# Performance work log

Measured on AMD Instinct MI355X. Metric: run time of the kernel, lower is better.

## Reference

```python
import jax, jax.numpy as jnp
import numpy as np

EPS = 1e-6


def _mp_match(reps, att, kernel):
    """BiMPM multi-perspective match.
    reps: (B,L,D); att: (B,L,D) or (B,1,D); kernel: (M,D).
    Returns (B,L,1+M): [tanh(sum(reps*att)), tanh(sum_d reps*kernel_m*att)].
    """
    prod = reps * att                                   # (B,L,D)
    cos = jnp.tanh(jnp.sum(prod, axis=-1, keepdims=True))   # (B,L,1)
    mp = jnp.tanh(jnp.einsum('bld,md->blm', prod, kernel))  # (B,L,M)
    return jnp.concatenate([cos, mp], axis=-1)


def setup_inputs() -> dict:
    key = jax.random.key(0)
    ks = jax.random.split(key, 12)
    B, Llt, Lrt, D, M, A = 32, 128, 128, 512, 64, 128
    H = D // 2
    u = lambda k, shape: jax.random.uniform(k, shape, jnp.float32, -0.05, 0.05)  # keras 'uniform' init
    return {
        'reps_lt': jax.random.normal(ks[0], (B, Llt, D), jnp.float32),
        'h_lt_fw': jax.random.normal(ks[1], (B, H), jnp.float32),
        'h_lt_bw': jax.random.normal(ks[2], (B, H), jnp.float32),
        'reps_rt': jax.random.normal(ks[3], (B, Lrt, D), jnp.float32),
        'h_rt_fw': jax.random.normal(ks[4], (B, H), jnp.float32),
        'h_rt_bw': jax.random.normal(ks[5], (B, H), jnp.float32),
        'kernel_full': u(ks[6], (M, D)),
        'kernel_mpool': u(ks[7], (M, D)),
        'attn_w1': u(ks[8], (D, A)),
        'diag_w': u(ks[9], (A,)),
        'kernel_att': u(ks[10], (M, D)),
        'kernel_maxatt': u(ks[11], (M, D)),
    }


def reference(reps_lt, h_lt_fw, h_lt_bw, reps_rt, h_rt_fw, h_rt_bw,
              kernel_full, kernel_mpool, attn_w1, diag_w,
              kernel_att, kernel_maxatt):
    # ---- full match: each left timestep vs last BiLSTM state of right ----
    h_rt = jnp.concatenate([h_rt_fw, h_rt_bw], axis=-1)[:, None, :]  # (B,1,D)
    full = _mp_match(reps_lt, h_rt, kernel_full)                     # (B,Ll,1+M)

    # ---- max-pooling match ----
    # t[b,r,l,m] = tanh(sum_d R[b,r,d]*K[m,d]*L[b,l,d]); max over right positions r
    r_scaled = jnp.einsum('brd,md->brmd', reps_rt, kernel_mpool)     # (B,Lr,M,D)
    t = jnp.tanh(jnp.einsum('brmd,bld->brlm', r_scaled, reps_lt))    # (B,Lr,Ll,M)
    mpool = jnp.max(t, axis=1)                                       # (B,Ll,M)

    # ---- attentive match ----
    a_lt = jnp.tanh(reps_lt @ attn_w1) * diag_w                      # (B,Ll,A)
    a_rt = jnp.tanh(reps_rt @ attn_w1)                               # (B,Lr,A)
    scores = jnp.einsum('bla,bra->blr', a_lt, a_rt)                  # (B,Ll,Lr)
    probs = jax.nn.softmax(scores, axis=-1)
    att = jnp.einsum('blr,brd->bld', probs, reps_rt)                 # (B,Ll,D)
    attentive = _mp_match(reps_lt, att, kernel_att)                  # (B,Ll,1+M)

    # ---- max-attentive match ----
    num = jnp.einsum('bld,brd->blr', reps_lt, reps_rt)
    n_lt = jnp.sqrt(jnp.maximum(jnp.sum(reps_lt * reps_lt, -1), EPS))[:, :, None]
    n_rt = jnp.sqrt(jnp.maximum(jnp.sum(reps_rt * reps_rt, -1), EPS))[:, None, :]
    rel = num / n_rt / n_lt                                          # (B,Ll,Lr)
    idx = jnp.argmax(rel, axis=2)                                    # (B,Ll) int
    max_att = jnp.take_along_axis(reps_rt, idx[:, :, None], axis=1)  # (B,Ll,D)
    maxatt = _mp_match(reps_lt, max_att, kernel_maxatt)              # (B,Ll,1+M)

    return jnp.concatenate([full, mpool, attentive, maxatt], axis=-1)  # (B,Ll,3+4M)
```

## Files before the change

### kernel.cpp

```cpp
#include <hip/hip_runtime.h>
#include <hip/hip_bf16.h>
#include <math.h>
#include <stdint.h>

typedef __attribute__((ext_vector_type(8))) short short8;
typedef __attribute__((ext_vector_type(4))) float float4v;

#define DEV static __device__ __forceinline__

DEV float bflo(unsigned int u) { union { unsigned int i; float f; } v; v.i = u << 16; return v.f; }
DEV float bfhi(unsigned int u) { union { unsigned int i; float f; } v; v.i = u & 0xffff0000u; return v.f; }
DEV unsigned short f2bf(float f) {
    union { float f; unsigned int i; } v; v.f = f;
    unsigned int x = v.i;
    return (unsigned short)((x + 0x7fffu + ((x >> 16) & 1u)) >> 16);
}
DEV unsigned int pack2(float a, float b) { return (unsigned int)f2bf(a) | ((unsigned int)f2bf(b) << 16); }
#if __has_builtin(__builtin_amdgcn_cvt_pk_bf16_f32)
DEV unsigned int pack2_fast(float a, float b) {
    typedef __attribute__((ext_vector_type(2))) short short2v;
    short2v r = __builtin_amdgcn_cvt_pk_bf16_f32(a, b);
    union { short2v s; unsigned int u; } v; v.s = r; return v.u;
}
#else
DEV unsigned int pack2_fast(float a, float b) { return pack2(a, b); }
#endif
DEV void unpack8(uint4 u, float* f) {
    f[0]=bflo(u.x); f[1]=bfhi(u.x); f[2]=bflo(u.y); f[3]=bfhi(u.y);
    f[4]=bflo(u.z); f[5]=bfhi(u.z); f[6]=bflo(u.w); f[7]=bfhi(u.w);
}

DEV void async16(const unsigned short* g, unsigned short* l) {
    __builtin_amdgcn_global_load_lds(
        (const __attribute__((address_space(1))) unsigned int*)g,
        (__attribute__((address_space(3))) unsigned int*)l, 16, 0, 0);
}

__global__ __launch_bounds__(256) void prep_kernel(const float* __restrict__ lt,
                                                   const float* __restrict__ rt,
                                                   const float* __restrict__ kf,
                                                   const float* __restrict__ kmp,
                                                   const float* __restrict__ ka,
                                                   const float* __restrict__ km,
                                                   const float* __restrict__ w1,
                                                   unsigned short* __restrict__ ltb,
                                                   unsigned short* __restrict__ rtb,
                                                   unsigned short* __restrict__ kb,
                                                   unsigned short* __restrict__ w1t,
                                                   unsigned short* __restrict__ rtbT,
                                                   double* __restrict__ rsq) {
    __shared__ double ws2[2][2];
    __shared__ float tile[32][33];
    int bid = blockIdx.x, t = threadIdx.x;
    if (bid < 1024) {
        bool isRt = bid >= 512;
        int base = (isRt ? (bid - 512) : bid) * 8;
        int rl = t >> 7;
        int c  = t & 127;
        const float* srcb = isRt ? rt : lt;
        unsigned short* dstb = isRt ? rtb : ltb;
        #pragma unroll
        for (int p = 0; p < 4; ++p) {
            int row = base + p * 2 + rl;
            const float* src = srcb + (size_t)row * 512;
            float4 v = *(const float4*)(src + c * 4);
            ushort4 o;
            o.x = f2bf(v.x); o.y = f2bf(v.y); o.z = f2bf(v.z); o.w = f2bf(v.w);
            *(ushort4*)(dstb + (size_t)row * 512 + c * 4) = o;
            if (isRt) {
                double s = (double)v.x * v.x + (double)v.y * v.y
                         + (double)v.z * v.z + (double)v.w * v.w;
                #pragma unroll
                for (int off = 1; off < 64; off <<= 1) s += __shfl_xor(s, off, 64);
                if ((c & 63) == 0) ws2[rl][c >> 6] = s;
                __syncthreads();
                if (c == 0) rsq[row] = 1.0 / sqrt(ws2[rl][0] + ws2[rl][1]);
                __syncthreads();
            }
        }
    } else if (bid < 1152) {
        int kbk = bid - 1024;
        int ksel = kbk >> 5;
        const float* src = (ksel == 0) ? kf : (ksel == 1) ? kmp : (ksel == 2) ? ka : km;
        int off = (kbk & 31) * 1024 + t * 4;
        float4 v = *(const float4*)(src + off);
        ushort4 o;
        o.x = f2bf(v.x); o.y = f2bf(v.y); o.z = f2bf(v.z); o.w = f2bf(v.w);
        *(ushort4*)(kb + ksel * 32768 + off) = o;
    } else if (bid < 1216) {
        int b2 = bid - 1152;
        int d0 = (b2 & 15) * 32, a0 = (b2 >> 4) * 32;
        int r = t >> 5, c = t & 31;
        #pragma unroll
        for (int i = 0; i < 32; i += 8)
            tile[r + i][c] = w1[(size_t)(d0 + r + i) * 128 + a0 + c];
        __syncthreads();
        #pragma unroll
        for (int i = 0; i < 32; i += 8)
            w1t[(size_t)(a0 + r + i) * 512 + d0 + c] = f2bf(tile[c][r + i]);
    } else {
        int b3 = bid - 1216;
        int b = b3 >> 6;
        int tid = b3 & 63;
        int d0 = (tid & 15) * 32;
        int r0 = (tid >> 4) * 32;
        int r = t >> 5, c = t & 31;
        #pragma unroll
        for (int i = 0; i < 32; i += 8)
            tile[r + i][c] = rt[(size_t)(b * 128 + r0 + r + i) * 512 + d0 + c];
        __syncthreads();
        #pragma unroll
        for (int i = 0; i < 32; i += 8)
            rtbT[(size_t)(b * 512 + d0 + r + i) * 128 + r0 + c] = f2bf(tile[c][r + i]);
    }
}

__global__ __launch_bounds__(256, 3) void uber_kernel(
        const unsigned short* __restrict__ ltb,
        const unsigned short* __restrict__ rtb,
        const unsigned short* __restrict__ kmb,
        const unsigned short* __restrict__ w1t,
        const float* __restrict__ diag,
        unsigned short* __restrict__ a_all,
        const double* __restrict__ rsq,
        unsigned int* __restrict__ candp,
        float* __restrict__ out) {
    __shared__ __align__(16) unsigned char smem[52224];
    int bx = blockIdx.x;
    int t = threadIdx.x;
    int wave = t >> 6, lane = t & 63;
    int q = lane >> 4, col = lane & 15, kq = q * 8;

    if (bx < 2048) {
        int xcd = bx & 7, jj = bx >> 3;
        int b = xcd * 4 + (jj >> 6);
        int m = jj & 63;
        unsigned short* ltS = (unsigned short*)smem;
        unsigned short* rtL = (unsigned short*)(smem + 16384);
        float (*mx)[2] = (float(*)[2])(smem + 16384 + 32768);
        int wl = wave & 1, wr = wave >> 1;
        const unsigned short* ltp = ltb + (size_t)b * 65536;
        const unsigned short* rtp = rtb + (size_t)b * 65536;
        const unsigned short* kr = kmb + (size_t)m * 512;
        int srow = t >> 3, cg8 = t & 7, cg = cg8 * 8;
        int gsw = (cg8 ^ (srow & 7)) * 8;
        int wbase = (t & ~63) * 8;

        #pragma unroll
        for (int it = 0; it < 4; ++it)
            async16(rtp + (size_t)(it * 32 + srow) * 512 + gsw,
                    rtL + it * 2048 + wbase);
        uint4 pk = *(const uint4*)(kr + cg);
        uint4 plt[4];
        #pragma unroll
        for (int it = 0; it < 4; ++it)
            plt[it] = *(const uint4*)(ltp + (size_t)(it * 32 + srow) * 512 + cg);

        float4v acc[4][4] = {};
        for (int k0i = 0; k0i < 8; ++k0i) {
            float kf8[8]; unpack8(pk, kf8);
            #pragma unroll
            for (int it = 0; it < 4; ++it) {
                int row = it * 32 + srow;
                float lf[8]; unpack8(plt[it], lf);
                uint4 s;
                s.x = pack2_fast(lf[0] * kf8[0], lf[1] * kf8[1]);
                s.y = pack2_fast(lf[2] * kf8[2], lf[3] * kf8[3]);
                s.z = pack2_fast(lf[4] * kf8[4], lf[5] * kf8[5]);
                s.w = pack2_fast(lf[6] * kf8[6], lf[7] * kf8[7]);
                *(uint4*)&ltS[row * 64 + gsw] = s;
            }
            __syncthreads();
            if (k0i < 7) {
                int k0n = (k0i + 1) * 64;
                int bofs = ((k0i + 1) & 1) * 8192;
                #pragma unroll
                for (int it = 0; it < 4; ++it)
                    async16(rtp + (size_t)(it * 32 + srow) * 512 + k0n + gsw,
                            rtL + bofs + it * 2048 + wbase);
                pk = *(const uint4*)(kr + k0n + cg);
                #pragma unroll
                for (int it = 0; it < 4; ++it)
                    plt[it] = *(const uint4*)(ltp + (size_t)(it * 32 + srow) * 512 + k0n + cg);
            }
            const unsigned short* rb = rtL + (k0i & 1) * 8192;
            #pragma unroll
            for (int kk = 0; kk < 64; kk += 32) {
                short8 af[4], bfr[4];
                #pragma unroll
                for (int i = 0; i < 4; ++i) {
                    int rowA = wl * 64 + i * 16 + col;
                    int slotA = ((kk >> 3) + q) ^ (rowA & 7);
                    af[i] = *(const short8*)&ltS[rowA * 64 + slotA * 8];
                }
                #pragma unroll
                for (int j = 0; j < 4; ++j) {
                    int row = wr * 64 + j * 16 + col;
                    int slot = ((kk >> 3) + q) ^ (row & 7);
                    bfr[j] = *(const short8*)&rb[row * 64 + slot * 8];
                }
                #pragma unroll
                for (int i = 0; i < 4; ++i)
                    #pragma unroll
                    for (int j = 0; j < 4; ++j)
                        acc[i][j] = __builtin_amdgcn_mfma_f32_16x16x32_bf16(af[i], bfr[j], acc[i][j], 0, 0, 0);
            }
            __syncthreads();
        }
        #pragma unroll
        for (int i = 0; i < 4; ++i)
            #pragma unroll
            for (int ii = 0; ii < 4; ++ii) {
                float v = fmaxf(fmaxf(acc[i][0][ii], acc[i][1][ii]), fmaxf(acc[i][2][ii], acc[i][3][ii]));
                #pragma unroll
                for (int off = 1; off < 16; off <<= 1) v = fmaxf(v, __shfl_xor(v, off, 64));
                if (col == 0) mx[wl * 64 + i * 16 + q * 4 + ii][wr] = v;
            }
        __syncthreads();
        if (t < 128)
            out[((size_t)(b * 128 + t)) * 259 + 65 + m] = tanhf(fmaxf(mx[t][0], mx[t][1]));

    } else if (bx < 2080) {
        int sb = bx - 2048;
        int xcd = sb & 7;
        int b = xcd * 4 + (sb >> 3);
        unsigned short* ltS = (unsigned short*)smem;
        unsigned short* rtL = (unsigned short*)(smem + 16384);
        float* rsqf = (float*)(smem + 49152);
        unsigned int (*candL)[2] = (unsigned int(*)[2])(smem + 49664);
        int wl = wave & 1, wr = wave >> 1;
        const unsigned short* ltp = ltb + (size_t)b * 65536;
        const unsigned short* rtp = rtb + (size_t)b * 65536;
        int srow = t >> 3, cg8 = t & 7, cg = cg8 * 8;
        int gsw = (cg8 ^ (srow & 7)) * 8;
        int wbase = (t & ~63) * 8;

        #pragma unroll
        for (int it = 0; it < 4; ++it)
            async16(rtp + (size_t)(it * 32 + srow) * 512 + gsw,
                    rtL + it * 2048 + wbase);
        uint4 plt[4];
        #pragma unroll
        for (int it = 0; it < 4; ++it)
            plt[it] = *(const uint4*)(ltp + (size_t)(it * 32 + srow) * 512 + cg);
        if (t < 128) rsqf[t] = (float)rsq[b * 128 + t];

        float4v acc[4][4] = {};
        for (int k0i = 0; k0i < 8; ++k0i) {
            #pragma unroll
            for (int it = 0; it < 4; ++it) {
                int row = it * 32 + srow;
                *(uint4*)&ltS[row * 64 + gsw] = plt[it];
            }
            __syncthreads();
            if (k0i < 7) {
                int k0n = (k0i + 1) * 64;
                int bofs = ((k0i + 1) & 1) * 8192;
                #pragma unroll
                for (int it = 0; it < 4; ++it)
                    async16(rtp + (size_t)(it * 32 + srow) * 512 + k0n + gsw,
                            rtL + bofs + it * 2048 + wbase);
                #pragma unroll
                for (int it = 0; it < 4; ++it)
                    plt[it] = *(const uint4*)(ltp + (size_t)(it * 32 + srow) * 512 + k0n + cg);
            }
            const unsigned short* rb = rtL + (k0i & 1) * 8192;
            #pragma unroll
            for (int kk = 0; kk < 64; kk += 32) {
                short8 af[4], bfr[4];
                #pragma unroll
                for (int i = 0; i < 4; ++i) {
                    int rowA = wl * 64 + i * 16 + col;
                    int slotA = ((kk >> 3) + q) ^ (rowA & 7);
                    af[i] = *(const short8*)&ltS[rowA * 64 + slotA * 8];
                }
                #pragma unroll
                for (int j = 0; j < 4; ++j) {
                    int row = wr * 64 + j * 16 + col;
                    int slot = ((kk >> 3) + q) ^ (row & 7);
                    bfr[j] = *(const short8*)&rb[row * 64 + slot * 8];
                }
                #pragma unroll
                for (int i = 0; i < 4; ++i)
                    #pragma unroll
                    for (int j = 0; j < 4; ++j)
                        acc[i][j] = __builtin_amdgcn_mfma_f32_16x16x32_bf16(af[i], bfr[j], acc[i][j], 0, 0, 0);
            }
            __syncthreads();
        }
        float rq[4];
        #pragma unroll
        for (int j = 0; j < 4; ++j) rq[j] = rsqf[wr * 64 + j * 16 + col];
        #pragma unroll
        for (int i = 0; i < 4; ++i)
            #pragma unroll
            for (int ii = 0; ii < 4; ++ii) {
                float v1 = -3.0e38f, v2 = -3.0e38f; int i1 = 0, i2 = 1;
                #pragma unroll
                for (int j = 0; j < 4; ++j) {
                    int rc = wr * 64 + j * 16 + col;
                    float s = acc[i][j][ii] * rq[j];
                    if (s > v1) { v2 = v1; i2 = i1; v1 = s; i1 = rc; }
                    else if (s > v2) { v2 = s; i2 = rc; }
                }
                #pragma unroll
                for (int off = 1; off < 16; off <<= 1) {
                    float u1 = __shfl_xor(v1, off, 64); int j1 = __shfl_xor(i1, off, 64);
                    float u2 = __shfl_xor(v2, off, 64); int j2 = __shfl_xor(i2, off, 64);
                    if (u1 > v1) {
                        float ov = v1; int oi = i1;
                        v1 = u1; i1 = j1;
                        if (u2 > ov) { v2 = u2; i2 = j2; } else { v2 = ov; i2 = oi; }
                    } else if (u1 > v2) { v2 = u1; i2 = j1; }
                }
                if (col == 0)
                    candL[wl * 64 + i * 16 + q * 4 + ii][wr] =
                        (unsigned int)i1 | ((unsigned int)i2 << 8);
            }
        __syncthreads();
        if (t < 128)
            candp[b * 128 + t] = candL[t][0] | (candL[t][1] << 16);

    } else {
        int R0 = (bx - 2080) * 32;
        unsigned short (*aS)[72] = (unsigned short(*)[72])smem;
        unsigned short (*bS)[72] = (unsigned short(*)[72])(smem + 4608);
        float* diagS = (float*)(smem + 4608 + 18432);
        int wl = wave & 1, wr = wave >> 1;
        if (t < 128) diagS[t] = diag[t];
        const unsigned short* src = (R0 < 4096) ? (ltb + (size_t)R0 * 512) : (rtb + (size_t)(R0 - 4096) * 512);
        float4v acc[4] = {};
        for (int k0 = 0; k0 < 512; k0 += 64) {
            {
                int row = t >> 3, cg = (t & 7) * 8;
                *(uint4*)&aS[row][cg] = *(const uint4*)(src + (size_t)row * 512 + k0 + cg);
            }
            #pragma unroll
            for (int it = 0; it < 4; ++it) {
                int id = it * 256 + t;
                int row = id >> 3, cg = (id & 7) * 8;
                *(uint4*)&bS[row][cg] = *(const uint4*)(w1t + (size_t)row * 512 + k0 + cg);
            }
            __syncthreads();
            #pragma unroll
            for (int kk = 0; kk < 64; kk += 32) {
                short8 af = *(const short8*)&aS[wl * 16 + col][kk + kq];
                #pragma unroll
                for (int j = 0; j < 4; ++j) {
                    short8 bf = *(const short8*)&bS[wr * 64 + j * 16 + col][kk + kq];
                    acc[j] = __builtin_amdgcn_mfma_f32_16x16x32_bf16(af, bf, acc[j], 0, 0, 0);
                }
            }
            __syncthreads();
        }
        bool isLt = (R0 < 4096);
        #pragma unroll
        for (int j = 0; j < 4; ++j)
            #pragma unroll
            for (int ii = 0; ii < 4; ++ii) {
                int rowl = wl * 16 + q * 4 + ii;
                int n = wr * 64 + j * 16 + col;
                float v = tanhf(acc[j][ii]);
                if (isLt) v *= diagS[n];
                a_all[((size_t)(R0 + rowl)) * 128 + n] = f2bf(v);
            }
    }
}

__global__ __launch_bounds__(512, 6) void tail_kernel(
        const unsigned short* __restrict__ a_all,
        const unsigned short* __restrict__ rtb,
        const unsigned short* __restrict__ rtbT,
        const float* __restrict__ ltf,
        const float* __restrict__ rtf,
        const double* __restrict__ rsq,
        const unsigned short* __restrict__ kb,
        const float* __restrict__ hfw,
        const float* __restrict__ hbw,
        const unsigned int* __restrict__ candp,
        float* __restrict__ out) {
    __shared__ __align__(16) unsigned char smem[53504];
    int bx = blockIdx.x;
    int t = threadIdx.x;
    int wave = t >> 6, lane = t & 63;
    int q = lane >> 4, col = lane & 15, kq = q * 8;

    if (bx < 256) {
        int b = bx & 31, lg = bx >> 5;
        int L0 = lg * 16;
        unsigned short (*altS)[136]  = (unsigned short(*)[136])(smem);
        unsigned short (*artS)[136]  = (unsigned short(*)[136])(smem + 4352);
        float (*pmax)[8] = (float(*)[8])(smem + 39168);
        float (*psum)[8] = (float(*)[8])(smem + 39680);
        const unsigned short* kb_att = kb + 2 * 32768;

        if (t < 256) {
            int row = t >> 4, c0 = (t & 15) * 8;
            *(uint4*)&altS[row][c0] = *(const uint4*)(a_all + ((size_t)(b * 128 + L0 + row)) * 128 + c0);
        }
        {
            int row = t >> 2, c0 = (t & 3) * 32;
            const unsigned short* src = a_all + ((size_t)(4096 + b * 128 + row)) * 128 + c0;
            #pragma unroll
            for (int i = 0; i < 4; ++i)
                *(uint4*)&artS[row][c0 + i * 8] = *(const uint4*)(src + i * 8);
        }
        __syncthreads();

        float4v acc = {};
        #pragma unroll
        for (int kk = 0; kk < 128; kk += 32) {
            short8 af = *(const short8*)&altS[col][kk + kq];
            short8 bf = *(const short8*)&artS[wave * 16 + col][kk + kq];
            acc = __builtin_amdgcn_mfma_f32_16x16x32_bf16(af, bf, acc, 0, 0, 0);
        }
        float m4[4], p4[4];
        #pragma unroll
        for (int ii = 0; ii < 4; ++ii) {
            float v = acc[ii];
            #pragma unroll
            for (int off = 1; off < 16; off <<= 1) v = fmaxf(v, __shfl_xor(v, off, 64));
            m4[ii] = v;
        }
        if (col == 0) {
            #pragma unroll
            for (int ii = 0; ii < 4; ++ii) pmax[q * 4 + ii][wave] = m4[ii];
        }
        __syncthreads();
        #pragma unroll
        for (int ii = 0; ii < 4; ++ii) {
            float M = pmax[q * 4 + ii][0];
            #pragma unroll
            for (int w = 1; w < 8; ++w) M = fmaxf(M, pmax[q * 4 + ii][w]);
            p4[ii] = expf(acc[ii] - M);
            float sv = p4[ii];
            #pragma unroll
            for (int off = 1; off < 16; off <<= 1) sv += __shfl_xor(sv, off, 64);
            m4[ii] = sv;
        }
        if (col == 0) {
            #pragma unroll
            for (int ii = 0; ii < 4; ++ii) psum[q * 4 + ii][wave] = m4[ii];
        }
        __syncthreads();
        unsigned short* Pb = (unsigned short*)smem;
        #pragma unroll
        for (int ii = 0; ii < 4; ++ii) {
            float S = psum[q * 4 + ii][0] + psum[q * 4 + ii][1] + psum[q * 4 + ii][2] + psum[q * 4 + ii][3]
                    + psum[q * 4 + ii][4] + psum[q * 4 + ii][5] + psum[q * 4 + ii][6] + psum[q * 4 + ii][7];
            Pb[(q * 4 + ii) * 136 + wave * 16 + col] = f2bf(p4[ii] / S);
        }

        unsigned short* Bc = (unsigned short*)(smem + 4352);
        float* attF = (float*)(smem + 20736);
        const unsigned short* rtT = rtbT + (size_t)b * 65536;
        for (int cc = 0; cc < 4; ++cc) {
            float4v pacc = {};
            for (int rh = 0; rh < 2; ++rh) {
                #pragma unroll
                for (int k = 0; k < 2; ++k) {
                    int id = (k * 8 + wave) * 64 + lane;
                    int row = id >> 3, grp = id & 7;
                    int d   = (row >> 4) * 64 + cc * 16 + (row & 15);
                    int sg  = grp ^ (row & 7);
                    async16(rtT + (size_t)d * 128 + rh * 64 + sg * 8,
                            Bc + (size_t)id * 8);
                }
                __syncthreads();
                #pragma unroll
                for (int ks = 0; ks < 2; ++ks) {
                    short8 afP = *(const short8*)&Pb[col * 136 + rh * 64 + ks * 32 + kq];
                    int rowB = wave * 16 + col;
                    short8 bfB = *(const short8*)&Bc[rowB * 64 + (((ks * 4 + q) ^ (rowB & 7)) * 8)];
                    pacc = __builtin_amdgcn_mfma_f32_16x16x32_bf16(afP, bfB, pacc, 0, 0, 0);
                }
                __syncthreads();
            }
            #pragma unroll
            for (int ii = 0; ii < 4; ++ii)
                attF[(q * 4 + ii) * 512 + wave * 64 + cc * 16 + col] = pacc[ii];
        }
        __syncthreads();

        int l = t >> 5, cd = t & 31;
        float a8[2][8];
        #pragma unroll
        for (int pass = 0; pass < 2; ++pass) {
            *(float4*)&a8[pass][0] = *(const float4*)&attF[l * 512 + pass * 256 + cd * 8];
            *(float4*)&a8[pass][4] = *(const float4*)&attF[l * 512 + pass * 256 + cd * 8 + 4];
        }
        __syncthreads();

        unsigned short (*prodsF)[520] = (unsigned short(*)[520])smem;
        unsigned short* Ks = (unsigned short*)(smem + 16640);
        float* red = (float*)(smem + 16640);

        int grow = b * 128 + L0 + l;
        const float* ltrow = ltf + (size_t)grow * 512;
        float csum = 0.f;
        #pragma unroll
        for (int pass = 0; pass < 2; ++pass) {
            int d0 = pass * 256 + cd * 8;
            float lf[8];
            *(float4*)&lf[0] = *(const float4*)(ltrow + d0);
            *(float4*)&lf[4] = *(const float4*)(ltrow + d0 + 4);
            float pf[8];
            #pragma unroll
            for (int k = 0; k < 8; ++k) { pf[k] = lf[k] * a8[pass][k]; csum += pf[k]; }
            uint4 o;
            o.x = pack2(pf[0], pf[1]); o.y = pack2(pf[2], pf[3]);
            o.z = pack2(pf[4], pf[5]); o.w = pack2(pf[6], pf[7]);
            *(uint4*)&prodsF[l][d0] = o;
        }
        #pragma unroll
        for (int off = 1; off < 32; off <<= 1) csum += __shfl_xor(csum, off, 64);
        if (cd == 0) out[(size_t)grow * 259 + 129] = tanhf(csum);

        for (int half = 0; half < 2; ++half) {
            __syncthreads();
            {
                int row = t >> 4, c0 = (t & 15) * 32;
                const unsigned short* src = kb_att + ((size_t)(half * 32 + row)) * 512 + c0;
                #pragma unroll
                for (int i = 0; i < 4; ++i)
                    *(uint4*)&Ks[row * 520 + c0 + i * 8] = *(const uint4*)(src + i * 8);
            }
            __syncthreads();
            float4v pacc[2] = {};
            #pragma unroll
            for (int kk = 0; kk < 64; kk += 32) {
                short8 af = *(const short8*)&prodsF[col][wave * 64 + kk + kq];
                #pragma unroll
                for (int j = 0; j < 2; ++j) {
                    short8 bf = *(const short8*)&Ks[(j * 16 + col) * 520 + wave * 64 + kk + kq];
                    pacc[j] = __builtin_amdgcn_mfma_f32_16x16x32_bf16(af, bf, pacc[j], 0, 0, 0);
                }
            }
            __syncthreads();
            #pragma unroll
            for (int j = 0; j < 2; ++j)
                #pragma unroll
                for (int ii = 0; ii < 4; ++ii)
                    red[((wave * 2 + j) * 16 + q * 4 + ii) * 16 + col] = pacc[j][ii];
            __syncthreads();
            {
                int ll = t >> 5, jm = t & 31;
                int j = jm >> 4, mc = jm & 15;
                float sv = 0.f;
                #pragma unroll
                for (int w = 0; w < 8; ++w) sv += red[((w * 2 + j) * 16 + ll) * 16 + mc];
                out[((size_t)(b * 128 + L0 + ll)) * 259 + 130 + half * 32 + jm] = tanhf(sv);
            }
        }

    } else {
        int idB = bx - 256;
        int lg = idB & 7, b = (idB >> 3) & 31;
        int mode = (idB >> 8) ? 2 : 0;
        int L0 = lg * 16;
        unsigned short (*prods)[520] = (unsigned short(*)[520])smem;
        unsigned short* Ks = (unsigned short*)(smem + 16640);
        float* red = (float*)(smem + 16640);
        double* dvs2 = (double*)(smem + 49920);
        int* idxl = (int*)(smem + 50432);
        const unsigned short* Kp = kb + (size_t)((mode == 0) ? 0 : 3 * 32768);
        int obase = (mode == 0) ? 0 : 194;

        if (mode == 2) {
            int dotid = t >> 3, sub = t & 7;
            int l = dotid >> 2, c = dotid & 3;
            unsigned int cpl = candp[b * 128 + L0 + l];
            int rr0 = (cpl >> (c * 8)) & 0xff;
            const float* lrow = ltf + ((size_t)(b * 128 + L0 + l)) * 512;
            const float* rrow = rtf + ((size_t)(b * 128 + rr0)) * 512;
            double sv = 0.0;
            #pragma unroll 8
            for (int k = 0; k < 64; ++k) {
                int d = sub * 64 + k;
                sv = fma((double)lrow[d], (double)rrow[d], sv);
            }
            #pragma unroll
            for (int off = 1; off < 8; off <<= 1) sv += __shfl_xor(sv, off, 64);
            if (sub == 0) dvs2[dotid] = sv * rsq[b * 128 + rr0];
            __syncthreads();
            if (t < 16) {
                unsigned int cl = candp[b * 128 + L0 + t];
                int bi = 256; double bv = -1.0e300;
                #pragma unroll
                for (int cc = 0; cc < 4; ++cc) {
                    int rr = (cl >> (cc * 8)) & 0xff;
                    double v = dvs2[t * 4 + cc];
                    if (v > bv || (v == bv && rr < bi)) { bv = v; bi = rr; }
                }
                idxl[t] = bi;
            }
            __syncthreads();
        }

        if (t < 256) {
            int l = t >> 4, c = t & 15;
            int grow = b * 128 + L0 + l;
            const float* ltrow = ltf + (size_t)grow * 512;
            const unsigned short* avrow = 0;
            if (mode == 2) avrow = rtb + ((size_t)(b * 128 + idxl[l])) * 512;
            float csum = 0.f;
            #pragma unroll
            for (int pass = 0; pass < 4; ++pass) {
                int d0 = pass * 128 + c * 8;
                float lf[8], af[8], pf[8];
                *(float4*)&lf[0] = *(const float4*)(ltrow + d0);
                *(float4*)&lf[4] = *(const float4*)(ltrow + d0 + 4);
                if (mode == 0) {
                    const float* h = (d0 < 256) ? (hfw + b * 256 + d0) : (hbw + b * 256 + d0 - 256);
                    *(float4*)&af[0] = *(const float4*)h;
                    *(float4*)&af[4] = *(const float4*)(h + 4);
                } else {
                    uint4 av = *(const uint4*)(avrow + d0);
                    unpack8(av, af);
                }
                #pragma unroll
                for (int k = 0; k < 8; ++k) { pf[k] = lf[k] * af[k]; csum += pf[k]; }
                uint4 o;
                o.x = pack2(pf[0], pf[1]); o.y = pack2(pf[2], pf[3]);
                o.z = pack2(pf[4], pf[5]); o.w = pack2(pf[6], pf[7]);
                *(uint4*)&prods[l][d0] = o;
            }
            #pragma unroll
            for (int off = 1; off < 16; off <<= 1) csum += __shfl_xor(csum, off, 64);
            if (c == 0) out[(size_t)grow * 259 + obase] = tanhf(csum);
        }
        for (int half = 0; half < 2; ++half) {
            if (half == 1) __syncthreads();
            {
                int row = t >> 4, c0 = (t & 15) * 32;
                const unsigned short* src = Kp + ((size_t)(half * 32 + row)) * 512 + c0;
                #pragma unroll
                for (int i = 0; i < 4; ++i)
                    *(uint4*)&Ks[row * 520 + c0 + i * 8] = *(const uint4*)(src + i * 8);
            }
            __syncthreads();
            float4v acc2[2] = {};
            #pragma unroll
            for (int kk = 0; kk < 64; kk += 32) {
                short8 af = *(const short8*)&prods[col][wave * 64 + kk + kq];
                #pragma unroll
                for (int j = 0; j < 2; ++j) {
                    short8 bf = *(const short8*)&Ks[(j * 16 + col) * 520 + wave * 64 + kk + kq];
                    acc2[j] = __builtin_amdgcn_mfma_f32_16x16x32_bf16(af, bf, acc2[j], 0, 0, 0);
                }
            }
            __syncthreads();
            #pragma unroll
            for (int j = 0; j < 2; ++j)
                #pragma unroll
                for (int ii = 0; ii < 4; ++ii)
                    red[((wave * 2 + j) * 16 + q * 4 + ii) * 16 + col] = acc2[j][ii];
            __syncthreads();
            {
                int ll = t >> 5, jm = t & 31;
                int j = jm >> 4, mc = jm & 15;
                float sv = 0.f;
                #pragma unroll
                for (int w = 0; w < 8; ++w) sv += red[((w * 2 + j) * 16 + ll) * 16 + mc];
                out[((size_t)(b * 128 + L0 + ll)) * 259 + obase + 1 + half * 32 + jm] = tanhf(sv);
            }
        }
    }
}

extern "C" void kernel_launch(void* const* d_in, const int* in_sizes, int n_in,
                              void* d_out, int out_size, void* d_ws, size_t ws_size,
                              hipStream_t stream) {
    const float* lt  = (const float*)d_in[0];
    const float* rt  = (const float*)d_in[3];
    const float* hfw = (const float*)d_in[4];
    const float* hbw = (const float*)d_in[5];
    const float* kf  = (const float*)d_in[6];
    const float* kmp = (const float*)d_in[7];
    const float* w1  = (const float*)d_in[8];
    const float* dia = (const float*)d_in[9];
    const float* ka  = (const float*)d_in[10];
    const float* km  = (const float*)d_in[11];
    float* out = (float*)d_out;

    char* wsb = (char*)d_ws;
    unsigned short* ltb16 = (unsigned short*)(wsb);
    unsigned short* rtb16 = (unsigned short*)(wsb + 4194304);
    unsigned short* kb16  = (unsigned short*)(wsb + 8388608);
    unsigned short* w1t   = (unsigned short*)(wsb + 8650752);
    unsigned short* a_all = (unsigned short*)(wsb + 8781824);
    unsigned short* rtbT  = (unsigned short*)(wsb + 10878976);
    double*         rsq   = (double*)(wsb + 15073280);
    unsigned int*   candp = (unsigned int*)(wsb + 15106048);

    prep_kernel<<<3264, 256, 0, stream>>>(lt, rt, kf, kmp, ka, km, w1, ltb16, rtb16, kb16, w1t, rtbT, rsq);
    uber_kernel<<<2336, 256, 0, stream>>>(ltb16, rtb16, kb16 + 32768, w1t, dia, a_all,
                                          rsq, candp, out);
    tail_kernel<<<768, 512, 0, stream>>>(a_all, rtb16, rtbT, lt, rt, rsq, kb16, hfw, hbw, candp, out);
}
```

Baseline: 175.7 us.

## Process two max-pool perspectives per block to reuse right-side tiles

```diff
diff --git a/kernel.cpp b/kernel.cpp
--- a/kernel.cpp
+++ b/kernel.cpp
@@ -115,7 +115,7 @@
     }
 }
 
-__global__ __launch_bounds__(256, 3) void uber_kernel(
+__global__ __launch_bounds__(256, 2) void uber_kernel(
         const unsigned short* __restrict__ ltb,
         const unsigned short* __restrict__ rtb,
         const unsigned short* __restrict__ kmb,
@@ -125,23 +125,24 @@
         const double* __restrict__ rsq,
         unsigned int* __restrict__ candp,
         float* __restrict__ out) {
-    __shared__ __align__(16) unsigned char smem[52224];
+    __shared__ __align__(16) unsigned char smem[65536];
     int bx = blockIdx.x;
     int t = threadIdx.x;
     int wave = t >> 6, lane = t & 63;
     int q = lane >> 4, col = lane & 15, kq = q * 8;
 
-    if (bx < 2048) {
+    if (bx < 1024) {
         int xcd = bx & 7, jj = bx >> 3;
-        int b = xcd * 4 + (jj >> 6);
-        int m = jj & 63;
-        unsigned short* ltS = (unsigned short*)smem;
-        unsigned short* rtL = (unsigned short*)(smem + 16384);
-        float (*mx)[2] = (float(*)[2])(smem + 16384 + 32768);
+        int b = xcd * 4 + (jj >> 5);
+        int m0 = (jj & 31) * 2;
+        unsigned short* ltS0 = (unsigned short*)smem;
+        unsigned short* ltS1 = (unsigned short*)(smem + 16384);
+        unsigned short* rtL  = (unsigned short*)(smem + 32768);
         int wl = wave & 1, wr = wave >> 1;
         const unsigned short* ltp = ltb + (size_t)b * 65536;
         const unsigned short* rtp = rtb + (size_t)b * 65536;
-        const unsigned short* kr = kmb + (size_t)m * 512;
+        const unsigned short* kr0 = kmb + (size_t)m0 * 512;
+        const unsigned short* kr1 = kmb + (size_t)(m0 + 1) * 512;
         int srow = t >> 3, cg8 = t & 7, cg = cg8 * 8;
         int gsw = (cg8 ^ (srow & 7)) * 8;
         int wbase = (t & ~63) * 8;
@@ -150,25 +151,33 @@
         for (int it = 0; it < 4; ++it)
             async16(rtp + (size_t)(it * 32 + srow) * 512 + gsw,
                     rtL + it * 2048 + wbase);
-        uint4 pk = *(const uint4*)(kr + cg);
+        uint4 pk0 = *(const uint4*)(kr0 + cg);
+        uint4 pk1 = *(const uint4*)(kr1 + cg);
         uint4 plt[4];
         #pragma unroll
         for (int it = 0; it < 4; ++it)
             plt[it] = *(const uint4*)(ltp + (size_t)(it * 32 + srow) * 512 + cg);
 
-        float4v acc[4][4] = {};
+        float4v acc0[4][4] = {};
+        float4v acc1[4][4] = {};
         for (int k0i = 0; k0i < 8; ++k0i) {
-            float kf8[8]; unpack8(pk, kf8);
+            float kf0[8]; unpack8(pk0, kf0);
+            float kf1[8]; unpack8(pk1, kf1);
             #pragma unroll
             for (int it = 0; it < 4; ++it) {
                 int row = it * 32 + srow;
                 float lf[8]; unpack8(plt[it], lf);
-                uint4 s;
-                s.x = pack2_fast(lf[0] * kf8[0], lf[1] * kf8[1]);
-                s.y = pack2_fast(lf[2] * kf8[2], lf[3] * kf8[3]);
-                s.z = pack2_fast(lf[4] * kf8[4], lf[5] * kf8[5]);
-                s.w = pack2_fast(lf[6] * kf8[6], lf[7] * kf8[7]);
-                *(uint4*)&ltS[row * 64 + gsw] = s;
+                uint4 s0, s1;
+                s0.x = pack2_fast(lf[0] * kf0[0], lf[1] * kf0[1]);
+                s0.y = pack2_fast(lf[2] * kf0[2], lf[3] * kf0[3]);
+                s0.z = pack2_fast(lf[4] * kf0[4], lf[5] * kf0[5]);
+                s0.w = pack2_fast(lf[6] * kf0[6], lf[7] * kf0[7]);
+                *(uint4*)&ltS0[row * 64 + gsw] = s0;
+                s1.x = pack2_fast(lf[0] * kf1[0], lf[1] * kf1[1]);
+                s1.y = pack2_fast(lf[2] * kf1[2], lf[3] * kf1[3]);
+                s1.z = pack2_fast(lf[4] * kf1[4], lf[5] * kf1[5]);
+                s1.w = pack2_fast(lf[6] * kf1[6], lf[7] * kf1[7]);
+                *(uint4*)&ltS1[row * 64 + gsw] = s1;
             }
             __syncthreads();
             if (k0i < 7) {
@@ -178,7 +187,8 @@
                 for (int it = 0; it < 4; ++it)
                     async16(rtp + (size_t)(it * 32 + srow) * 512 + k0n + gsw,
                             rtL + bofs + it * 2048 + wbase);
-                pk = *(const uint4*)(kr + k0n + cg);
+                pk0 = *(const uint4*)(kr0 + k0n + cg);
+                pk1 = *(const uint4*)(kr1 + k0n + cg);
                 #pragma unroll
                 for (int it = 0; it < 4; ++it)
                     plt[it] = *(const uint4*)(ltp + (size_t)(it * 32 + srow) * 512 + k0n + cg);
@@ -186,12 +196,13 @@
             const unsigned short* rb = rtL + (k0i & 1) * 8192;
             #pragma unroll
             for (int kk = 0; kk < 64; kk += 32) {
-                short8 af[4], bfr[4];
+                short8 af0[4], af1[4], bfr[4];
                 #pragma unroll
                 for (int i = 0; i < 4; ++i) {
                     int rowA = wl * 64 + i * 16 + col;
                     int slotA = ((kk >> 3) + q) ^ (rowA & 7);
-                    af[i] = *(const short8*)&ltS[rowA * 64 + slotA * 8];
+                    af0[i] = *(const short8*)&ltS0[rowA * 64 + slotA * 8];
+                    af1[i] = *(const short8*)&ltS1[rowA * 64 + slotA * 8];
                 }
                 #pragma unroll
                 for (int j = 0; j < 4; ++j) {
@@ -202,26 +213,40 @@
                 #pragma unroll
                 for (int i = 0; i < 4; ++i)
                     #pragma unroll
-                    for (int j = 0; j < 4; ++j)
-                        acc[i][j] = __builtin_amdgcn_mfma_f32_16x16x32_bf16(af[i], bfr[j], acc[i][j], 0, 0, 0);
-            }
-            __syncthreads();
-        }
+                    for (int j = 0; j < 4; ++j) {
+                        acc0[i][j] = __builtin_amdgcn_mfma_f32_16x16x32_bf16(af0[i], bfr[j], acc0[i][j], 0, 0, 0);
+                        acc1[i][j] = __builtin_amdgcn_mfma_f32_16x16x32_bf16(af1[i], bfr[j], acc1[i][j], 0, 0, 0);
+                    }
+            }
+            __syncthreads();
+        }
+        float (*mx0)[2] = (float(*)[2])smem;
+        float (*mx1)[2] = (float(*)[2])(smem + 1024);
         #pragma unroll
         for (int i = 0; i < 4; ++i)
             #pragma unroll
             for (int ii = 0; ii < 4; ++ii) {
-                float v = fmaxf(fmaxf(acc[i][0][ii], acc[i][1][ii]), fmaxf(acc[i][2][ii], acc[i][3][ii]));
-                #pragma unroll
-                for (int off = 1; off < 16; off <<= 1) v = fmaxf(v, __shfl_xor(v, off, 64));
-                if (col == 0) mx[wl * 64 + i * 16 + q * 4 + ii][wr] = v;
-            }
-        __syncthreads();
-        if (t < 128)
-            out[((size_t)(b * 128 + t)) * 259 + 65 + m] = tanhf(fmaxf(mx[t][0], mx[t][1]));
-
-    } else if (bx < 2080) {
-        int sb = bx - 2048;
+                float v0 = fmaxf(fmaxf(acc0[i][0][ii], acc0[i][1][ii]), fmaxf(acc0[i][2][ii], acc0[i][3][ii]));
+                float v1 = fmaxf(fmaxf(acc1[i][0][ii], acc1[i][1][ii]), fmaxf(acc1[i][2][ii], acc1[i][3][ii]));
+                #pragma unroll
+                for (int off = 1; off < 16; off <<= 1) {
+                    v0 = fmaxf(v0, __shfl_xor(v0, off, 64));
+                    v1 = fmaxf(v1, __shfl_xor(v1, off, 64));
+                }
+                if (col == 0) {
+                    mx0[wl * 64 + i * 16 + q * 4 + ii][wr] = v0;
+                    mx1[wl * 64 + i * 16 + q * 4 + ii][wr] = v1;
+                }
+            }
+        __syncthreads();
+        if (t < 128) {
+            size_t orow = ((size_t)(b * 128 + t)) * 259 + 65;
+            out[orow + m0]     = tanhf(fmaxf(mx0[t][0], mx0[t][1]));
+            out[orow + m0 + 1] = tanhf(fmaxf(mx1[t][0], mx1[t][1]));
+        }
+
+    } else if (bx < 1056) {
+        int sb = bx - 1024;
         int xcd = sb & 7;
         int b = xcd * 4 + (sb >> 3);
         unsigned short* ltS = (unsigned short*)smem;
@@ -322,7 +347,7 @@
             candp[b * 128 + t] = candL[t][0] | (candL[t][1] << 16);
 
     } else {
-        int R0 = (bx - 2080) * 32;
+        int R0 = (bx - 1056) * 32;
         unsigned short (*aS)[72] = (unsigned short(*)[72])smem;
         unsigned short (*bS)[72] = (unsigned short(*)[72])(smem + 4608);
         float* diagS = (float*)(smem + 4608 + 18432);
@@ -694,7 +719,7 @@
     unsigned int*   candp = (unsigned int*)(wsb + 15106048);
 
     prep_kernel<<<3264, 256, 0, stream>>>(lt, rt, kf, kmp, ka, km, w1, ltb16, rtb16, kb16, w1t, rtbT, rsq);
-    uber_kernel<<<2336, 256, 0, stream>>>(ltb16, rtb16, kb16 + 32768, w1t, dia, a_all,
+    uber_kernel<<<1312, 256, 0, stream>>>(ltb16, rtb16, kb16 + 32768, w1t, dia, a_all,
                                           rsq, candp, out);
     tail_kernel<<<768, 512, 0, stream>>>(a_all, rtb16, rtbT, lt, rt, rsq, kb16, hfw, hbw, candp, out);
 }
```

After: 171.8 us. -2.2%, faster.
